# Kernel optimization log

Hardware: AMD Instinct MI355X
Metric: run time of the kernel (lower is better)

## Reference

```python
import jax, jax.numpy as jnp
import numpy as np

TAGSET = 128
START = 126
END = 127
NEG = -10000.0


def setup_inputs() -> dict:
    key = jax.random.key(0)
    k1, k2, k3 = jax.random.split(key, 3)
    B, S, T = 256, 512, TAGSET
    feats = jax.random.normal(k1, (B, S, T), dtype=jnp.float32)
    tags = jax.random.randint(k2, (B, S), 0, 126, dtype=jnp.int64)
    mask = jnp.ones((B, S), dtype=jnp.int32)
    # learned transitions with hard constraints baked in, as in __init__
    transitions = jax.random.normal(k3, (T, T), dtype=jnp.float32)
    transitions = transitions.at[START, :].set(NEG)
    transitions = transitions.at[:, END].set(NEG)
    return {"feats": feats, "tags": tags, "mask": mask, "transitions": transitions}


def _gold_score(feats, tags, mask_f, transitions):
    B, S, T = feats.shape
    tags_ext = jnp.concatenate(
        [jnp.full((B, 1), START, dtype=tags.dtype), tags], axis=1)  # (B, S+1)
    prev_t = tags_ext[:, :-1]
    cur_t = tags_ext[:, 1:]
    trans = transitions[prev_t, cur_t]                               # (B, S)
    emit = jnp.take_along_axis(feats, cur_t[:, :, None], axis=2)[..., 0]
    score = jnp.sum((trans + emit) * mask_f, axis=1)                 # (B,)
    # tag at last valid position (index mask.sum into start-prepended tags)
    lengths = jnp.sum(mask_f, axis=1).astype(jnp.int32)             # (B,)
    last_tags = jnp.take_along_axis(tags_ext, lengths[:, None].astype(tags.dtype), axis=1)[:, 0]
    return score + transitions[last_tags, END]


def _log_partition(feats, transitions):
    # NOTE: original code's mask application in the forward recursion is a
    # no-op (alpha*mask + alpha*~mask), so the recurrence runs over all steps.
    B, S, T = feats.shape
    log_alpha0 = jnp.full((B, T), NEG, dtype=feats.dtype).at[:, START].set(0.0)

    def step(log_alpha, feat_t):
        # score[b, j, k] = alpha[b, k] + transitions[j, k] + feat_t[b, j]
        s = log_alpha[:, None, :] + transitions[None, :, :] + feat_t[:, :, None]
        return jax.nn.logsumexp(s, axis=2), None

    log_alpha, _ = jax.lax.scan(step, log_alpha0, jnp.swapaxes(feats, 0, 1))
    log_alpha = log_alpha + transitions[:, END][None, :]
    return jax.nn.logsumexp(log_alpha, axis=1)                       # (B,)


def reference(feats, tags, mask, transitions):
    mask_f = mask.astype(feats.dtype)
    score = _gold_score(feats, tags, mask_f, transitions)
    log_z = _log_partition(feats, transitions)
    return -(score - log_z)  # per-example NLL, shape (B,)
```

## Files before the change

kernel.cpp:

```cpp
#include <hip/hip_runtime.h>
#include <stdint.h>

#define T_ 128
#define S_ 512
#define STARTT 126
#define ENDT 127

typedef float f32x4 __attribute__((ext_vector_type(4)));
typedef __bf16 bf16x8 __attribute__((ext_vector_type(8)));

union BFU { unsigned short s[8]; bf16x8 v; };

__device__ __forceinline__ unsigned short bf16r(float f) {
  unsigned int x = __float_as_uint(f);
  x += 0x7fffu + ((x >> 16) & 1u);
  return (unsigned short)(x >> 16);
}

__global__ __launch_bounds__(512)
void crf_fused(const float* __restrict__ feats,
               const int* __restrict__ tags,
               const int* __restrict__ mask,
               const float* __restrict__ trans,
               float* __restrict__ out)
{
  const int b    = blockIdx.x;
  const int tid  = threadIdx.x;
  const int lane = tid & 63;
  const int w    = tid >> 6;
  const int dir  = (w >= 4);
  const int wd   = w & 3;

  __shared__ __align__(16) float tstage[T_ * T_];
  __shared__ float red_s[8];
  __shared__ float red_l[8];
  __shared__ float sc_final;
  __shared__ __align__(16) unsigned short ubuf[2][2][T_];
  __shared__ float h0buf[2][2];
  __shared__ float hfF[T_], hfB[T_];
  __shared__ float cshare[2];

  const float* fb = feats + (size_t)b * (S_ * T_);

  {
    const f32x4* src = (const f32x4*)trans;
    f32x4* dst = (f32x4*)tstage;
    #pragma unroll
    for (int i = 0; i < 8; ++i) dst[tid + 512 * i] = src[tid + 512 * i];
  }
  __syncthreads();

  {
    int s = tid;
    int cur  = tags[b * S_ + s];
    int prev = (s == 0) ? STARTT : tags[b * S_ + s - 1];
    float mk = (float)mask[b * S_ + s];
    float sc = (tstage[prev * T_ + cur] + fb[s * T_ + cur]) * mk;
    float ln = mk;
    #pragma unroll
    for (int off = 32; off; off >>= 1) {
      sc += __shfl_down(sc, off);
      ln += __shfl_down(ln, off);
    }
    if (lane == 0) { red_s[w] = sc; red_l[w] = ln; }
  }
  __syncthreads();
  if (tid == 0) {
    float sc = 0.f, ln = 0.f;
    #pragma unroll
    for (int i = 0; i < 8; ++i) { sc += red_s[i]; ln += red_l[i]; }
    int L = (int)ln;
    int last = (L == 0) ? STARTT : tags[b * S_ + L - 1];
    sc_final = sc + tstage[last * T_ + ENDT];
  }

  const int n_ = lane & 15;
  const int g_ = lane >> 4;
  bf16x8 Bf0[4], Bf1[4];
  #pragma unroll
  for (int tt = 0; tt < 2; ++tt) {
    #pragma unroll
    for (int c = 0; c < 4; ++c) {
      BFU u_;
      #pragma unroll
      for (int e = 0; e < 8; ++e) {
        int kk = 32 * c + 8 * g_ + e;
        int nn = 16 * (2 * wd + tt) + n_;
        int row = dir ? kk : nn;
        int col = dir ? nn : kk;
        u_.s[e] = bf16r(__expf(tstage[row * T_ + col]));
      }
      if (tt == 0) Bf0[c] = u_.v; else Bf1[c] = u_.v;
    }
  }

  const int jf = 32 * wd + (lane & 31);
  const int rs = dir ? -T_ : T_;
  const float* fpD = fb + jf + (dir ? (511 * T_) : 0);
  float f0 = fpD[0];
  float f1 = fpD[1 * rs];
  float f2 = fpD[2 * rs];
  float f3 = fpD[3 * rs];
  float f4 = fpD[4 * rs];
  float f5 = fpD[5 * rs];
  float f6 = fpD[6 * rs];
  float f7 = fpD[7 * rs];

  float Ctot = 0.f;
  float hv;

  if (!dir) {
    float tv = tstage[jf * T_ + STARTT];
    hv = f0 + fmaxf(tv, -69.0f);
  } else {
    hv = 0.f;
  }
  {
    float uu = __expf(dir ? (hv + f0) : hv);
    if (lane < 32) ubuf[dir][1][jf] = bf16r(uu);
    if (lane == 0 && wd == 0) h0buf[dir][1] = 0.f;
  }
  f0 = fpD[8 * rs];
  asm volatile("s_waitcnt lgkmcnt(0)" ::: "memory");
  __builtin_amdgcn_s_barrier();

#define CRF_STEP(KK, FR) do {                                                  \
    const int par_ = (KK) & 1;                                                 \
    float h0p = h0buf[dir][par_];                                              \
    const unsigned short* ub_ = &ubuf[dir][par_][0];                           \
    bf16x8 A0 = *(const bf16x8*)(ub_ +       8 * g_);                          \
    bf16x8 A1 = *(const bf16x8*)(ub_ + 32 +  8 * g_);                          \
    bf16x8 A2 = *(const bf16x8*)(ub_ + 64 +  8 * g_);                          \
    bf16x8 A3 = *(const bf16x8*)(ub_ + 96 +  8 * g_);                          \
    f32x4 ac0 = {0.f, 0.f, 0.f, 0.f};                                          \
    f32x4 ac1 = ac0, ac2 = ac0, ac3 = ac0;                                     \
    ac0 = __builtin_amdgcn_mfma_f32_16x16x32_bf16(A0, Bf0[0], ac0, 0, 0, 0);   \
    ac2 = __builtin_amdgcn_mfma_f32_16x16x32_bf16(A0, Bf1[0], ac2, 0, 0, 0);   \
    ac1 = __builtin_amdgcn_mfma_f32_16x16x32_bf16(A1, Bf0[1], ac1, 0, 0, 0);   \
    ac3 = __builtin_amdgcn_mfma_f32_16x16x32_bf16(A1, Bf1[1], ac3, 0, 0, 0);   \
    ac0 = __builtin_amdgcn_mfma_f32_16x16x32_bf16(A2, Bf0[2], ac0, 0, 0, 0);   \
    ac2 = __builtin_amdgcn_mfma_f32_16x16x32_bf16(A2, Bf1[2], ac2, 0, 0, 0);   \
    ac1 = __builtin_amdgcn_mfma_f32_16x16x32_bf16(A3, Bf0[3], ac1, 0, 0, 0);   \
    ac3 = __builtin_amdgcn_mfma_f32_16x16x32_bf16(A3, Bf1[3], ac3, 0, 0, 0);   \
    float Sv = (lane & 16) ? (ac2[0] + ac3[0]) : (ac0[0] + ac1[0]);            \
    Sv = fmaxf(Sv, 1e-30f);                                                    \
    float lg_ = __logf(Sv) - h0p;                                              \
    hv = dir ? lg_ : ((FR) + lg_);                                             \
    Ctot += h0p;                                                               \
    float uu_ = __expf(dir ? (hv + (FR)) : hv);                                \
    if (lane < 32) ubuf[dir][par_ ^ 1][jf] = bf16r(uu_);                       \
    if (lane == 0 && wd == 0) h0buf[dir][par_ ^ 1] = hv;                       \
    if ((KK) + 8 <= 255) FR = fpD[((KK) + 8) * rs];                            \
    asm volatile("s_waitcnt lgkmcnt(0)" ::: "memory");                         \
    __builtin_amdgcn_s_barrier();                                              \
} while (0)

  #pragma unroll 1
  for (int k0 = 1; k0 <= 241; k0 += 8) {
    CRF_STEP(k0 + 0, f1); CRF_STEP(k0 + 1, f2); CRF_STEP(k0 + 2, f3); CRF_STEP(k0 + 3, f4);
    CRF_STEP(k0 + 4, f5); CRF_STEP(k0 + 5, f6); CRF_STEP(k0 + 6, f7); CRF_STEP(k0 + 7, f0);
  }
  CRF_STEP(249, f1); CRF_STEP(250, f2); CRF_STEP(251, f3); CRF_STEP(252, f4);
  CRF_STEP(253, f5); CRF_STEP(254, f6); CRF_STEP(255, f7);

  if (dir) {
    float h0p = h0buf[1][0];
    const unsigned short* ub_ = &ubuf[1][0][0];
    bf16x8 A0 = *(const bf16x8*)(ub_ +       8 * g_);
    bf16x8 A1 = *(const bf16x8*)(ub_ + 32 +  8 * g_);
    bf16x8 A2 = *(const bf16x8*)(ub_ + 64 +  8 * g_);
    bf16x8 A3 = *(const bf16x8*)(ub_ + 96 +  8 * g_);
    f32x4 ac0 = {0.f, 0.f, 0.f, 0.f};
    f32x4 ac1 = ac0, ac2 = ac0, ac3 = ac0;
    ac0 = __builtin_amdgcn_mfma_f32_16x16x32_bf16(A0, Bf0[0], ac0, 0, 0, 0);
    ac2 = __builtin_amdgcn_mfma_f32_16x16x32_bf16(A0, Bf1[0], ac2, 0, 0, 0);
    ac1 = __builtin_amdgcn_mfma_f32_16x16x32_bf16(A1, Bf0[1], ac1, 0, 0, 0);
    ac3 = __builtin_amdgcn_mfma_f32_16x16x32_bf16(A1, Bf1[1], ac3, 0, 0, 0);
    ac0 = __builtin_amdgcn_mfma_f32_16x16x32_bf16(A2, Bf0[2], ac0, 0, 0, 0);
    ac2 = __builtin_amdgcn_mfma_f32_16x16x32_bf16(A2, Bf1[2], ac2, 0, 0, 0);
    ac1 = __builtin_amdgcn_mfma_f32_16x16x32_bf16(A3, Bf0[3], ac1, 0, 0, 0);
    ac3 = __builtin_amdgcn_mfma_f32_16x16x32_bf16(A3, Bf1[3], ac3, 0, 0, 0);
    float Sv = (lane & 16) ? (ac2[0] + ac3[0]) : (ac0[0] + ac1[0]);
    Sv = fmaxf(Sv, 1e-30f);
    hv = __logf(Sv) - h0p;
    Ctot += h0p;
  }

  if (lane < 32) {
    if (!dir) hfF[jf] = hv; else hfB[jf] = hv;
  }
  if (tid == 0)   cshare[0] = Ctot;
  if (tid == 256) cshare[1] = Ctot;
  __syncthreads();
  if (tid < 64) {
    float a  = hfF[tid]      + hfB[tid];
    float b2 = hfF[tid + 64] + hfB[tid + 64];
    float M = fmaxf(a, b2);
    #pragma unroll
    for (int off = 32; off; off >>= 1) M = fmaxf(M, __shfl_xor(M, off));
    float sm = __expf(a - M) + __expf(b2 - M);
    #pragma unroll
    for (int off = 32; off; off >>= 1) sm += __shfl_xor(sm, off);
    if (tid == 0) {
      float logz = cshare[0] + cshare[1] + M + __logf(sm) - 10000.0f;
      out[b] = logz - sc_final;
    }
  }
#undef CRF_STEP
}

extern "C" void kernel_launch(void* const* d_in, const int* in_sizes, int n_in,
                              void* d_out, int out_size, void* d_ws, size_t ws_size,
                              hipStream_t stream) {
  const float* feats = (const float*)d_in[0];
  const int*   tags  = (const int*)d_in[1];
  const int*   mask  = (const int*)d_in[2];
  const float* trans = (const float*)d_in[3];
  float* out = (float*)d_out;
  hipLaunchKernelGGL(crf_fused, dim3(256), dim3(512), 0, stream,
                     feats, tags, mask, trans, out);
}
```

Baseline: 92.72 us.

## Merge forward/backward into same waves with power-of-two exp-domain rescaling

```diff
diff --git a/kernel.cpp b/kernel.cpp
--- a/kernel.cpp
+++ b/kernel.cpp
@@ -16,8 +16,14 @@
   x += 0x7fffu + ((x >> 16) & 1u);
   return (unsigned short)(x >> 16);
 }
-
-__global__ __launch_bounds__(512)
+__device__ __forceinline__ int expbits(float x) {
+  return (int)((__float_as_uint(x) >> 23) & 0xffu);
+}
+__device__ __forceinline__ float scalef(int k) {
+  return __uint_as_float((unsigned)(318 - k) << 23);
+}
+
+__global__ __launch_bounds__(256)
 void crf_fused(const float* __restrict__ feats,
                const int* __restrict__ tags,
                const int* __restrict__ mask,
@@ -28,17 +34,12 @@
   const int tid  = threadIdx.x;
   const int lane = tid & 63;
   const int w    = tid >> 6;
-  const int dir  = (w >= 4);
-  const int wd   = w & 3;
 
   __shared__ __align__(16) float tstage[T_ * T_];
-  __shared__ float red_s[8];
-  __shared__ float red_l[8];
+  __shared__ float red_s[4], red_l[4], redd[4];
   __shared__ float sc_final;
   __shared__ __align__(16) unsigned short ubuf[2][2][T_];
-  __shared__ float h0buf[2][2];
-  __shared__ float hfF[T_], hfB[T_];
-  __shared__ float cshare[2];
+  __shared__ __align__(8) int kbuf[2][2];
 
   const float* fb = feats + (size_t)b * (S_ * T_);
 
@@ -46,17 +47,21 @@
     const f32x4* src = (const f32x4*)trans;
     f32x4* dst = (f32x4*)tstage;
     #pragma unroll
-    for (int i = 0; i < 8; ++i) dst[tid + 512 * i] = src[tid + 512 * i];
+    for (int i = 0; i < 16; ++i) dst[tid + 256 * i] = src[tid + 256 * i];
   }
   __syncthreads();
 
   {
-    int s = tid;
-    int cur  = tags[b * S_ + s];
-    int prev = (s == 0) ? STARTT : tags[b * S_ + s - 1];
-    float mk = (float)mask[b * S_ + s];
-    float sc = (tstage[prev * T_ + cur] + fb[s * T_ + cur]) * mk;
-    float ln = mk;
+    float sc = 0.f, ln = 0.f;
+    #pragma unroll
+    for (int it = 0; it < 2; ++it) {
+      int s = tid + 256 * it;
+      int cur  = tags[b * S_ + s];
+      int prev = (s == 0) ? STARTT : tags[b * S_ + s - 1];
+      float mk = (float)mask[b * S_ + s];
+      sc += (tstage[prev * T_ + cur] + fb[s * T_ + cur]) * mk;
+      ln += mk;
+    }
     #pragma unroll
     for (int off = 32; off; off >>= 1) {
       sc += __shfl_down(sc, off);
@@ -68,7 +73,7 @@
   if (tid == 0) {
     float sc = 0.f, ln = 0.f;
     #pragma unroll
-    for (int i = 0; i < 8; ++i) { sc += red_s[i]; ln += red_l[i]; }
+    for (int i = 0; i < 4; ++i) { sc += red_s[i]; ln += red_l[i]; }
     int L = (int)ln;
     int last = (L == 0) ? STARTT : tags[b * S_ + L - 1];
     sc_final = sc + tstage[last * T_ + ENDT];
@@ -76,137 +81,164 @@
 
   const int n_ = lane & 15;
   const int g_ = lane >> 4;
-  bf16x8 Bf0[4], Bf1[4];
-  #pragma unroll
-  for (int tt = 0; tt < 2; ++tt) {
-    #pragma unroll
-    for (int c = 0; c < 4; ++c) {
-      BFU u_;
-      #pragma unroll
-      for (int e = 0; e < 8; ++e) {
-        int kk = 32 * c + 8 * g_ + e;
-        int nn = 16 * (2 * wd + tt) + n_;
-        int row = dir ? kk : nn;
-        int col = dir ? nn : kk;
-        u_.s[e] = bf16r(__expf(tstage[row * T_ + col]));
-      }
-      if (tt == 0) Bf0[c] = u_.v; else Bf1[c] = u_.v;
-    }
-  }
-
-  const int jf = 32 * wd + (lane & 31);
-  const int rs = dir ? -T_ : T_;
-  const float* fpD = fb + jf + (dir ? (511 * T_) : 0);
-  float f0 = fpD[0];
-  float f1 = fpD[1 * rs];
-  float f2 = fpD[2 * rs];
-  float f3 = fpD[3 * rs];
-  float f4 = fpD[4 * rs];
-  float f5 = fpD[5 * rs];
-  float f6 = fpD[6 * rs];
-  float f7 = fpD[7 * rs];
-
-  float Ctot = 0.f;
-  float hv;
-
-  if (!dir) {
-    float tv = tstage[jf * T_ + STARTT];
-    hv = f0 + fmaxf(tv, -69.0f);
-  } else {
-    hv = 0.f;
-  }
-  {
-    float uu = __expf(dir ? (hv + f0) : hv);
-    if (lane < 32) ubuf[dir][1][jf] = bf16r(uu);
-    if (lane == 0 && wd == 0) h0buf[dir][1] = 0.f;
-  }
-  f0 = fpD[8 * rs];
+  bf16x8 BF0[4], BF1[4], BB0[4], BB1[4];
+
+#define BUILDFRAG(DST, ROW_IS_K, TT) do {                                      \
+    _Pragma("unroll")                                                          \
+    for (int c = 0; c < 4; ++c) {                                              \
+      BFU u_;                                                                  \
+      _Pragma("unroll")                                                        \
+      for (int e = 0; e < 8; ++e) {                                            \
+        int kk = 32 * c + 8 * g_ + e;                                          \
+        int nn = 16 * (2 * w + (TT)) + n_;                                     \
+        int row = (ROW_IS_K) ? kk : nn;                                        \
+        int col = (ROW_IS_K) ? nn : kk;                                        \
+        u_.s[e] = bf16r(__expf(tstage[row * T_ + col]));                       \
+      }                                                                        \
+      DST[c] = u_.v;                                                           \
+    }                                                                          \
+  } while (0)
+
+  BUILDFRAG(BF0, 0, 0);  BUILDFRAG(BF1, 0, 1);
+  BUILDFRAG(BB0, 1, 0);  BUILDFRAG(BB1, 1, 1);
+#undef BUILDFRAG
+
+  const int jf = 32 * w + (lane & 31);
+  const bool lhalf = (lane < 32);
+  const bool selhi = (lane & 16) != 0;
+  const float* fpF = fb + jf;
+  const float* fpB = fb + jf + 511 * T_;
+  float fF0 = fpF[0 * T_], fF1 = fpF[1 * T_], fF2 = fpF[2 * T_], fF3 = fpF[3 * T_];
+  float fF4 = fpF[4 * T_], fF5 = fpF[5 * T_], fF6 = fpF[6 * T_], fF7 = fpF[7 * T_];
+  float fB0 = fpB[0], fB1 = fpB[-1 * T_], fB2 = fpB[-2 * T_], fB3 = fpB[-3 * T_];
+  float fB4 = fpB[-4 * T_], fB5 = fpB[-5 * T_], fB6 = fpB[-6 * T_], fB7 = fpB[-7 * T_];
+
+  int ksumF = 0, ksumB = 0;
+  float lastF = 0.f;
+
+  {
+    float trS = tstage[jf * T_ + STARTT];
+    float uF = __expf(fF0 + trS);
+    float uB = __expf(fB0);
+    if (lhalf) {
+      ubuf[0][1][jf] = bf16r(uF);
+      ubuf[1][1][jf] = bf16r(uB);
+    }
+    if (tid == 0) {
+      int2 kw; kw.x = expbits(uF); kw.y = expbits(uB);
+      *(int2*)&kbuf[1][0] = kw;
+    }
+    fF0 = fpF[8 * T_];
+    fB0 = fpB[-8 * T_];
+  }
   asm volatile("s_waitcnt lgkmcnt(0)" ::: "memory");
   __builtin_amdgcn_s_barrier();
 
-#define CRF_STEP(KK, FR) do {                                                  \
-    const int par_ = (KK) & 1;                                                 \
-    float h0p = h0buf[dir][par_];                                              \
-    const unsigned short* ub_ = &ubuf[dir][par_][0];                           \
-    bf16x8 A0 = *(const bf16x8*)(ub_ +       8 * g_);                          \
-    bf16x8 A1 = *(const bf16x8*)(ub_ + 32 +  8 * g_);                          \
-    bf16x8 A2 = *(const bf16x8*)(ub_ + 64 +  8 * g_);                          \
-    bf16x8 A3 = *(const bf16x8*)(ub_ + 96 +  8 * g_);                          \
-    f32x4 ac0 = {0.f, 0.f, 0.f, 0.f};                                          \
-    f32x4 ac1 = ac0, ac2 = ac0, ac3 = ac0;                                     \
-    ac0 = __builtin_amdgcn_mfma_f32_16x16x32_bf16(A0, Bf0[0], ac0, 0, 0, 0);   \
-    ac2 = __builtin_amdgcn_mfma_f32_16x16x32_bf16(A0, Bf1[0], ac2, 0, 0, 0);   \
-    ac1 = __builtin_amdgcn_mfma_f32_16x16x32_bf16(A1, Bf0[1], ac1, 0, 0, 0);   \
-    ac3 = __builtin_amdgcn_mfma_f32_16x16x32_bf16(A1, Bf1[1], ac3, 0, 0, 0);   \
-    ac0 = __builtin_amdgcn_mfma_f32_16x16x32_bf16(A2, Bf0[2], ac0, 0, 0, 0);   \
-    ac2 = __builtin_amdgcn_mfma_f32_16x16x32_bf16(A2, Bf1[2], ac2, 0, 0, 0);   \
-    ac1 = __builtin_amdgcn_mfma_f32_16x16x32_bf16(A3, Bf0[3], ac1, 0, 0, 0);   \
-    ac3 = __builtin_amdgcn_mfma_f32_16x16x32_bf16(A3, Bf1[3], ac3, 0, 0, 0);   \
-    float Sv = (lane & 16) ? (ac2[0] + ac3[0]) : (ac0[0] + ac1[0]);            \
-    Sv = fmaxf(Sv, 1e-30f);                                                    \
-    float lg_ = __logf(Sv) - h0p;                                              \
-    hv = dir ? lg_ : ((FR) + lg_);                                             \
-    Ctot += h0p;                                                               \
-    float uu_ = __expf(dir ? (hv + (FR)) : hv);                                \
-    if (lane < 32) ubuf[dir][par_ ^ 1][jf] = bf16r(uu_);                       \
-    if (lane == 0 && wd == 0) h0buf[dir][par_ ^ 1] = hv;                       \
-    if ((KK) + 8 <= 255) FR = fpD[((KK) + 8) * rs];                            \
+#define STEP_BODY(KK, FF, FB, DOPF) do {                                       \
+    const int par = (KK) & 1;                                                  \
+    int2 kk2 = *(const int2*)&kbuf[par][0];                                    \
+    const unsigned short* uf  = &ubuf[0][par][0];                              \
+    const unsigned short* ub2 = &ubuf[1][par][0];                              \
+    bf16x8 AF0 = *(const bf16x8*)(uf  +       8 * g_);                         \
+    bf16x8 AF1 = *(const bf16x8*)(uf  + 32 +  8 * g_);                         \
+    bf16x8 AF2 = *(const bf16x8*)(uf  + 64 +  8 * g_);                         \
+    bf16x8 AF3 = *(const bf16x8*)(uf  + 96 +  8 * g_);                         \
+    bf16x8 AB0 = *(const bf16x8*)(ub2 +       8 * g_);                         \
+    bf16x8 AB1 = *(const bf16x8*)(ub2 + 32 +  8 * g_);                         \
+    bf16x8 AB2 = *(const bf16x8*)(ub2 + 64 +  8 * g_);                         \
+    bf16x8 AB3 = *(const bf16x8*)(ub2 + 96 +  8 * g_);                         \
+    float mF = __expf(FF) * scalef(kk2.x);                                     \
+    float mB = __expf(FB) * scalef(kk2.y);                                     \
+    f32x4 aF0 = {0.f,0.f,0.f,0.f}; f32x4 aF1 = aF0, aF2 = aF0, aF3 = aF0;      \
+    f32x4 aB0 = aF0, aB1 = aF0, aB2 = aF0, aB3 = aF0;                          \
+    aF0 = __builtin_amdgcn_mfma_f32_16x16x32_bf16(AF0, BF0[0], aF0, 0, 0, 0);  \
+    aF2 = __builtin_amdgcn_mfma_f32_16x16x32_bf16(AF0, BF1[0], aF2, 0, 0, 0);  \
+    aF1 = __builtin_amdgcn_mfma_f32_16x16x32_bf16(AF1, BF0[1], aF1, 0, 0, 0);  \
+    aF3 = __builtin_amdgcn_mfma_f32_16x16x32_bf16(AF1, BF1[1], aF3, 0, 0, 0);  \
+    aF0 = __builtin_amdgcn_mfma_f32_16x16x32_bf16(AF2, BF0[2], aF0, 0, 0, 0);  \
+    aF2 = __builtin_amdgcn_mfma_f32_16x16x32_bf16(AF2, BF1[2], aF2, 0, 0, 0);  \
+    aF1 = __builtin_amdgcn_mfma_f32_16x16x32_bf16(AF3, BF0[3], aF1, 0, 0, 0);  \
+    aF3 = __builtin_amdgcn_mfma_f32_16x16x32_bf16(AF3, BF1[3], aF3, 0, 0, 0);  \
+    aB0 = __builtin_amdgcn_mfma_f32_16x16x32_bf16(AB0, BB0[0], aB0, 0, 0, 0);  \
+    aB2 = __builtin_amdgcn_mfma_f32_16x16x32_bf16(AB0, BB1[0], aB2, 0, 0, 0);  \
+    aB1 = __builtin_amdgcn_mfma_f32_16x16x32_bf16(AB1, BB0[1], aB1, 0, 0, 0);  \
+    aB3 = __builtin_amdgcn_mfma_f32_16x16x32_bf16(AB1, BB1[1], aB3, 0, 0, 0);  \
+    aB0 = __builtin_amdgcn_mfma_f32_16x16x32_bf16(AB2, BB0[2], aB0, 0, 0, 0);  \
+    aB2 = __builtin_amdgcn_mfma_f32_16x16x32_bf16(AB2, BB1[2], aB2, 0, 0, 0);  \
+    aB1 = __builtin_amdgcn_mfma_f32_16x16x32_bf16(AB3, BB0[3], aB1, 0, 0, 0);  \
+    aB3 = __builtin_amdgcn_mfma_f32_16x16x32_bf16(AB3, BB1[3], aB3, 0, 0, 0);  \
+    float SvF = selhi ? (aF2[0] + aF3[0]) : (aF0[0] + aF1[0]);                 \
+    float uFn = SvF * mF;                                                      \
+    float SvB = selhi ? (aB2[0] + aB3[0]) : (aB0[0] + aB1[0]);                 \
+    float uBn = SvB * mB;                                                      \
+    if (lhalf) {                                                               \
+      ubuf[0][par ^ 1][jf] = bf16r(uFn);                                       \
+      ubuf[1][par ^ 1][jf] = bf16r(uBn);                                       \
+    }                                                                          \
+    if (tid == 0) {                                                            \
+      int2 kw; kw.x = expbits(uFn); kw.y = expbits(uBn);                       \
+      *(int2*)&kbuf[par ^ 1][0] = kw;                                          \
+    }                                                                          \
+    ksumF += kk2.x; ksumB += kk2.y;                                            \
+    lastF = uFn;                                                               \
+    if (DOPF) {                                                                \
+      FF = fpF[((KK) + 8) * T_];                                               \
+      FB = fpB[-(((KK) + 8) * T_)];                                            \
+    }                                                                          \
     asm volatile("s_waitcnt lgkmcnt(0)" ::: "memory");                         \
     __builtin_amdgcn_s_barrier();                                              \
-} while (0)
+  } while (0)
+
+#define STEP(KK, FF, FB)  STEP_BODY(KK, FF, FB, 1)
+#define STEPN(KK, FF, FB) STEP_BODY(KK, FF, FB, 0)
 
   #pragma unroll 1
-  for (int k0 = 1; k0 <= 241; k0 += 8) {
-    CRF_STEP(k0 + 0, f1); CRF_STEP(k0 + 1, f2); CRF_STEP(k0 + 2, f3); CRF_STEP(k0 + 3, f4);
-    CRF_STEP(k0 + 4, f5); CRF_STEP(k0 + 5, f6); CRF_STEP(k0 + 6, f7); CRF_STEP(k0 + 7, f0);
-  }
-  CRF_STEP(249, f1); CRF_STEP(250, f2); CRF_STEP(251, f3); CRF_STEP(252, f4);
-  CRF_STEP(253, f5); CRF_STEP(254, f6); CRF_STEP(255, f7);
-
-  if (dir) {
-    float h0p = h0buf[1][0];
-    const unsigned short* ub_ = &ubuf[1][0][0];
-    bf16x8 A0 = *(const bf16x8*)(ub_ +       8 * g_);
-    bf16x8 A1 = *(const bf16x8*)(ub_ + 32 +  8 * g_);
-    bf16x8 A2 = *(const bf16x8*)(ub_ + 64 +  8 * g_);
-    bf16x8 A3 = *(const bf16x8*)(ub_ + 96 +  8 * g_);
-    f32x4 ac0 = {0.f, 0.f, 0.f, 0.f};
-    f32x4 ac1 = ac0, ac2 = ac0, ac3 = ac0;
-    ac0 = __builtin_amdgcn_mfma_f32_16x16x32_bf16(A0, Bf0[0], ac0, 0, 0, 0);
-    ac2 = __builtin_amdgcn_mfma_f32_16x16x32_bf16(A0, Bf1[0], ac2, 0, 0, 0);
-    ac1 = __builtin_amdgcn_mfma_f32_16x16x32_bf16(A1, Bf0[1], ac1, 0, 0, 0);
-    ac3 = __builtin_amdgcn_mfma_f32_16x16x32_bf16(A1, Bf1[1], ac3, 0, 0, 0);
-    ac0 = __builtin_amdgcn_mfma_f32_16x16x32_bf16(A2, Bf0[2], ac0, 0, 0, 0);
-    ac2 = __builtin_amdgcn_mfma_f32_16x16x32_bf16(A2, Bf1[2], ac2, 0, 0, 0);
-    ac1 = __builtin_amdgcn_mfma_f32_16x16x32_bf16(A3, Bf0[3], ac1, 0, 0, 0);
-    ac3 = __builtin_amdgcn_mfma_f32_16x16x32_bf16(A3, Bf1[3], ac3, 0, 0, 0);
-    float Sv = (lane & 16) ? (ac2[0] + ac3[0]) : (ac0[0] + ac1[0]);
-    Sv = fmaxf(Sv, 1e-30f);
-    hv = __logf(Sv) - h0p;
-    Ctot += h0p;
-  }
-
-  if (lane < 32) {
-    if (!dir) hfF[jf] = hv; else hfB[jf] = hv;
-  }
-  if (tid == 0)   cshare[0] = Ctot;
-  if (tid == 256) cshare[1] = Ctot;
+  for (int k0 = 1; k0 <= 233; k0 += 8) {
+    STEP(k0 + 0, fF1, fB1); STEP(k0 + 1, fF2, fB2);
+    STEP(k0 + 2, fF3, fB3); STEP(k0 + 3, fF4, fB4);
+    STEP(k0 + 4, fF5, fB5); STEP(k0 + 5, fF6, fB6);
+    STEP(k0 + 6, fF7, fB7); STEP(k0 + 7, fF0, fB0);
+  }
+  STEP (241, fF1, fB1); STEP (242, fF2, fB2); STEP (243, fF3, fB3);
+  STEP (244, fF4, fB4); STEP (245, fF5, fB5); STEP (246, fF6, fB6);
+  STEP (247, fF7, fB7); STEPN(248, fF0, fB0);
+  STEPN(249, fF1, fB1); STEPN(250, fF2, fB2); STEPN(251, fF3, fB3);
+  STEPN(252, fF4, fB4); STEPN(253, fF5, fB5); STEPN(254, fF6, fB6);
+  STEPN(255, fF7, fB7);
+
+#undef STEP
+#undef STEPN
+#undef STEP_BODY
+
+  {
+    const unsigned short* ub2 = &ubuf[1][0][0];
+    bf16x8 AB0 = *(const bf16x8*)(ub2 +       8 * g_);
+    bf16x8 AB1 = *(const bf16x8*)(ub2 + 32 +  8 * g_);
+    bf16x8 AB2 = *(const bf16x8*)(ub2 + 64 +  8 * g_);
+    bf16x8 AB3 = *(const bf16x8*)(ub2 + 96 +  8 * g_);
+    f32x4 aB0 = {0.f,0.f,0.f,0.f}; f32x4 aB1 = aB0, aB2 = aB0, aB3 = aB0;
+    aB0 = __builtin_amdgcn_mfma_f32_16x16x32_bf16(AB0, BB0[0], aB0, 0, 0, 0);
+    aB2 = __builtin_amdgcn_mfma_f32_16x16x32_bf16(AB0, BB1[0], aB2, 0, 0, 0);
+    aB1 = __builtin_amdgcn_mfma_f32_16x16x32_bf16(AB1, BB0[1], aB1, 0, 0, 0);
+    aB3 = __builtin_amdgcn_mfma_f32_16x16x32_bf16(AB1, BB1[1], aB3, 0, 0, 0);
+    aB0 = __builtin_amdgcn_mfma_f32_16x16x32_bf16(AB2, BB0[2], aB0, 0, 0, 0);
+    aB2 = __builtin_amdgcn_mfma_f32_16x16x32_bf16(AB2, BB1[2], aB2, 0, 0, 0);
+    aB1 = __builtin_amdgcn_mfma_f32_16x16x32_bf16(AB3, BB0[3], aB1, 0, 0, 0);
+    aB3 = __builtin_amdgcn_mfma_f32_16x16x32_bf16(AB3, BB1[3], aB3, 0, 0, 0);
+    float SvB = selhi ? (aB2[0] + aB3[0]) : (aB0[0] + aB1[0]);
+    float d = lhalf ? (lastF * 0x1p-64f) * (SvB * 0x1p-64f) : 0.f;
+    #pragma unroll
+    for (int off = 32; off; off >>= 1) d += __shfl_down(d, off);
+    if (lane == 0) redd[w] = d;
+  }
   __syncthreads();
-  if (tid < 64) {
-    float a  = hfF[tid]      + hfB[tid];
-    float b2 = hfF[tid + 64] + hfB[tid + 64];
-    float M = fmaxf(a, b2);
-    #pragma unroll
-    for (int off = 32; off; off >>= 1) M = fmaxf(M, __shfl_xor(M, off));
-    float sm = __expf(a - M) + __expf(b2 - M);
-    #pragma unroll
-    for (int off = 32; off; off >>= 1) sm += __shfl_xor(sm, off);
-    if (tid == 0) {
-      float logz = cshare[0] + cshare[1] + M + __logf(sm) - 10000.0f;
-      out[b] = logz - sc_final;
-    }
-  }
-#undef CRF_STEP
+  if (tid == 0) {
+    float dot = redd[0] + redd[1] + redd[2] + redd[3];
+    float logz = __logf(dot)
+               + (float)(ksumF + ksumB - 2 * 255 * 191 + 128) * 0.69314718056f
+               - 10000.0f;
+    out[b] = logz - sc_final;
+  }
 }
 
 extern "C" void kernel_launch(void* const* d_in, const int* in_sizes, int n_in,
@@ -217,6 +249,6 @@
   const int*   mask  = (const int*)d_in[2];
   const float* trans = (const float*)d_in[3];
   float* out = (float*)d_out;
-  hipLaunchKernelGGL(crf_fused, dim3(256), dim3(512), 0, stream,
+  hipLaunchKernelGGL(crf_fused, dim3(256), dim3(256), 0, stream,
                      feats, tags, mask, trans, out);
 }
```

After: 96.63 us. 4.2% more time.

## Run each CRF direction in a single wave using bpermute and exponent scaling

Applied to the files above, without the earlier changes.

```diff
diff --git a/kernel.cpp b/kernel.cpp
--- a/kernel.cpp
+++ b/kernel.cpp
@@ -9,6 +9,7 @@
 typedef float f32x4 __attribute__((ext_vector_type(4)));
 typedef __bf16 bf16x8 __attribute__((ext_vector_type(8)));
 
+union ABU { int i[4]; bf16x8 v; };
 union BFU { unsigned short s[8]; bf16x8 v; };
 
 __device__ __forceinline__ unsigned short bf16r(float f) {
@@ -16,8 +17,16 @@
   x += 0x7fffu + ((x >> 16) & 1u);
   return (unsigned short)(x >> 16);
 }
-
-__global__ __launch_bounds__(512)
+__device__ __forceinline__ float scalef(int k) {
+  return __uint_as_float((unsigned)(318 - k) << 23);
+}
+__device__ __forceinline__ unsigned cvt_pk_bf16(float lo, float hi) {
+  unsigned r;
+  asm("v_cvt_pk_bf16_f32 %0, %1, %2" : "=v"(r) : "v"(lo), "v"(hi));
+  return r;
+}
+
+__global__ __launch_bounds__(128, 1)
 void crf_fused(const float* __restrict__ feats,
                const int* __restrict__ tags,
                const int* __restrict__ mask,
@@ -28,17 +37,15 @@
   const int tid  = threadIdx.x;
   const int lane = tid & 63;
   const int w    = tid >> 6;
-  const int dir  = (w >= 4);
-  const int wd   = w & 3;
+  const int dir  = w;
+  const int cl   = lane & 15;
+  const int g    = lane >> 4;
 
   __shared__ __align__(16) float tstage[T_ * T_];
-  __shared__ float red_s[8];
-  __shared__ float red_l[8];
+  __shared__ float red_s[2], red_l[2];
+  __shared__ float fin_uf[T_], fin_w[T_];
+  __shared__ int   kls[2];
   __shared__ float sc_final;
-  __shared__ __align__(16) unsigned short ubuf[2][2][T_];
-  __shared__ float h0buf[2][2];
-  __shared__ float hfF[T_], hfB[T_];
-  __shared__ float cshare[2];
 
   const float* fb = feats + (size_t)b * (S_ * T_);
 
@@ -46,17 +53,21 @@
     const f32x4* src = (const f32x4*)trans;
     f32x4* dst = (f32x4*)tstage;
     #pragma unroll
-    for (int i = 0; i < 8; ++i) dst[tid + 512 * i] = src[tid + 512 * i];
+    for (int i = 0; i < 32; ++i) dst[tid + 128 * i] = src[tid + 128 * i];
   }
   __syncthreads();
 
   {
-    int s = tid;
-    int cur  = tags[b * S_ + s];
-    int prev = (s == 0) ? STARTT : tags[b * S_ + s - 1];
-    float mk = (float)mask[b * S_ + s];
-    float sc = (tstage[prev * T_ + cur] + fb[s * T_ + cur]) * mk;
-    float ln = mk;
+    float sc = 0.f, ln = 0.f;
+    #pragma unroll
+    for (int it = 0; it < 4; ++it) {
+      int s = tid + 128 * it;
+      int cur  = tags[b * S_ + s];
+      int prev = s ? tags[b * S_ + s - 1] : STARTT;
+      float mk = (float)mask[b * S_ + s];
+      sc += (tstage[prev * T_ + cur] + fb[s * T_ + cur]) * mk;
+      ln += mk;
+    }
     #pragma unroll
     for (int off = 32; off; off >>= 1) {
       sc += __shfl_down(sc, off);
@@ -66,147 +77,173 @@
   }
   __syncthreads();
   if (tid == 0) {
-    float sc = 0.f, ln = 0.f;
-    #pragma unroll
-    for (int i = 0; i < 8; ++i) { sc += red_s[i]; ln += red_l[i]; }
+    float sc = red_s[0] + red_s[1];
+    float ln = red_l[0] + red_l[1];
     int L = (int)ln;
-    int last = (L == 0) ? STARTT : tags[b * S_ + L - 1];
+    int last = L ? tags[b * S_ + L - 1] : STARTT;
     sc_final = sc + tstage[last * T_ + ENDT];
   }
 
-  const int n_ = lane & 15;
-  const int g_ = lane >> 4;
-  bf16x8 Bf0[4], Bf1[4];
+  bf16x8 Bfr[8][4];
   #pragma unroll
-  for (int tt = 0; tt < 2; ++tt) {
+  for (int t = 0; t < 8; ++t) {
     #pragma unroll
     for (int c = 0; c < 4; ++c) {
-      BFU u_;
+      BFU bu;
       #pragma unroll
       for (int e = 0; e < 8; ++e) {
-        int kk = 32 * c + 8 * g_ + e;
-        int nn = 16 * (2 * wd + tt) + n_;
-        int row = dir ? kk : nn;
-        int col = dir ? nn : kk;
-        u_.s[e] = bf16r(__expf(tstage[row * T_ + col]));
+        int ktag = 32 * (e >> 1) + 16 * (e & 1) + 4 * c + g;
+        int nn = 16 * t + cl;
+        float tv = dir ? tstage[ktag * T_ + nn] : tstage[nn * T_ + ktag];
+        bu.s[e] = bf16r(__expf(tv));
       }
-      if (tt == 0) Bf0[c] = u_.v; else Bf1[c] = u_.v;
-    }
-  }
-
-  const int jf = 32 * wd + (lane & 31);
+      Bfr[t][c] = bu.v;
+    }
+  }
+
+  int bp0 = (0 + g) * 4, bp1 = (4 + g) * 4, bp2 = (8 + g) * 4, bp3 = (12 + g) * 4;
+
   const int rs = dir ? -T_ : T_;
-  const float* fpD = fb + jf + (dir ? (511 * T_) : 0);
-  float f0 = fpD[0];
-  float f1 = fpD[1 * rs];
-  float f2 = fpD[2 * rs];
-  float f3 = fpD[3 * rs];
-  float f4 = fpD[4 * rs];
-  float f5 = fpD[5 * rs];
-  float f6 = fpD[6 * rs];
-  float f7 = fpD[7 * rs];
-
-  float Ctot = 0.f;
-  float hv;
+  const float* frow1 = fb + (dir ? 510 * T_ : 1 * T_) + cl;
+  float fr0[8], fr1[8], fr2[8], fr3[8];
+  #pragma unroll
+  for (int t = 0; t < 8; ++t) {
+    fr0[t] = frow1[0 * rs + 16 * t];
+    fr1[t] = frow1[1 * rs + 16 * t];
+    fr2[t] = frow1[2 * rs + 16 * t];
+    fr3[t] = frow1[3 * rs + 16 * t];
+  }
+  const float* fpl = frow1 + 4 * rs;
+
+  float u8v[8];
+  {
+    const float* f0p = fb + (dir ? 511 * T_ : 0) + cl;
+    #pragma unroll
+    for (int t = 0; t < 8; ++t) {
+      float fv = f0p[16 * t];
+      float tv = dir ? 0.f : tstage[(16 * t + cl) * T_ + STARTT];
+      u8v[t] = __expf(fv + tv);
+    }
+  }
+  int kexp = (__builtin_amdgcn_readlane((int)__float_as_uint(u8v[0]), 0) >> 23) & 255;
+  int ksum = kexp;
+  float scale = scalef(kexp);
+
+  ABU af[4];
+  {
+    unsigned Q0 = cvt_pk_bf16(u8v[0], u8v[1]);
+    unsigned Q1 = cvt_pk_bf16(u8v[2], u8v[3]);
+    unsigned Q2 = cvt_pk_bf16(u8v[4], u8v[5]);
+    unsigned Q3 = cvt_pk_bf16(u8v[6], u8v[7]);
+    af[0].i[0] = __builtin_amdgcn_ds_bpermute(bp0, (int)Q0);
+    af[0].i[1] = __builtin_amdgcn_ds_bpermute(bp0, (int)Q1);
+    af[0].i[2] = __builtin_amdgcn_ds_bpermute(bp0, (int)Q2);
+    af[0].i[3] = __builtin_amdgcn_ds_bpermute(bp0, (int)Q3);
+    af[1].i[0] = __builtin_amdgcn_ds_bpermute(bp1, (int)Q0);
+    af[1].i[1] = __builtin_amdgcn_ds_bpermute(bp1, (int)Q1);
+    af[1].i[2] = __builtin_amdgcn_ds_bpermute(bp1, (int)Q2);
+    af[1].i[3] = __builtin_amdgcn_ds_bpermute(bp1, (int)Q3);
+    af[2].i[0] = __builtin_amdgcn_ds_bpermute(bp2, (int)Q0);
+    af[2].i[1] = __builtin_amdgcn_ds_bpermute(bp2, (int)Q1);
+    af[2].i[2] = __builtin_amdgcn_ds_bpermute(bp2, (int)Q2);
+    af[2].i[3] = __builtin_amdgcn_ds_bpermute(bp2, (int)Q3);
+    af[3].i[0] = __builtin_amdgcn_ds_bpermute(bp3, (int)Q0);
+    af[3].i[1] = __builtin_amdgcn_ds_bpermute(bp3, (int)Q1);
+    af[3].i[2] = __builtin_amdgcn_ds_bpermute(bp3, (int)Q2);
+    af[3].i[3] = __builtin_amdgcn_ds_bpermute(bp3, (int)Q3);
+  }
+
+#define STEP(FR, UPD, PF) do {                                                   \
+    f32x4 z4 = {0.f, 0.f, 0.f, 0.f};                                             \
+    float S8[8];                                                                  \
+    _Pragma("unroll")                                                             \
+    for (int t = 0; t < 8; ++t) {                                                 \
+      f32x4 aA = __builtin_amdgcn_mfma_f32_16x16x32_bf16(af[0].v, Bfr[t][0], z4, 0, 0, 0); \
+      aA = __builtin_amdgcn_mfma_f32_16x16x32_bf16(af[1].v, Bfr[t][1], aA, 0, 0, 0);       \
+      f32x4 aB = __builtin_amdgcn_mfma_f32_16x16x32_bf16(af[2].v, Bfr[t][2], z4, 0, 0, 0); \
+      aB = __builtin_amdgcn_mfma_f32_16x16x32_bf16(af[3].v, Bfr[t][3], aB, 0, 0, 0);       \
+      S8[t] = aA[0] + aB[0];                                                      \
+    }                                                                             \
+    _Pragma("unroll")                                                             \
+    for (int t = 0; t < 8; ++t) u8v[t] = S8[t] * scale * __expf(FR[t]);           \
+    if (UPD) {                                                                    \
+      kexp = (__builtin_amdgcn_readlane((int)__float_as_uint(u8v[0]), 0) >> 23) & 255; \
+      ksum += kexp;                                                               \
+      scale = scalef(kexp);                                                       \
+    }                                                                             \
+    unsigned Q0 = cvt_pk_bf16(u8v[0], u8v[1]);                                    \
+    unsigned Q1 = cvt_pk_bf16(u8v[2], u8v[3]);                                    \
+    unsigned Q2 = cvt_pk_bf16(u8v[4], u8v[5]);                                    \
+    unsigned Q3 = cvt_pk_bf16(u8v[6], u8v[7]);                                    \
+    af[0].i[0] = __builtin_amdgcn_ds_bpermute(bp0, (int)Q0);                      \
+    af[0].i[1] = __builtin_amdgcn_ds_bpermute(bp0, (int)Q1);                      \
+    af[0].i[2] = __builtin_amdgcn_ds_bpermute(bp0, (int)Q2);                      \
+    af[0].i[3] = __builtin_amdgcn_ds_bpermute(bp0, (int)Q3);                      \
+    af[1].i[0] = __builtin_amdgcn_ds_bpermute(bp1, (int)Q0);                      \
+    af[1].i[1] = __builtin_amdgcn_ds_bpermute(bp1, (int)Q1);                      \
+    af[1].i[2] = __builtin_amdgcn_ds_bpermute(bp1, (int)Q2);                      \
+    af[1].i[3] = __builtin_amdgcn_ds_bpermute(bp1, (int)Q3);                      \
+    af[2].i[0] = __builtin_amdgcn_ds_bpermute(bp2, (int)Q0);                      \
+    af[2].i[1] = __builtin_amdgcn_ds_bpermute(bp2, (int)Q1);                      \
+    af[2].i[2] = __builtin_amdgcn_ds_bpermute(bp2, (int)Q2);                      \
+    af[2].i[3] = __builtin_amdgcn_ds_bpermute(bp2, (int)Q3);                      \
+    af[3].i[0] = __builtin_amdgcn_ds_bpermute(bp3, (int)Q0);                      \
+    af[3].i[1] = __builtin_amdgcn_ds_bpermute(bp3, (int)Q1);                      \
+    af[3].i[2] = __builtin_amdgcn_ds_bpermute(bp3, (int)Q2);                      \
+    af[3].i[3] = __builtin_amdgcn_ds_bpermute(bp3, (int)Q3);                      \
+    if (PF) {                                                                     \
+      _Pragma("unroll")                                                           \
+      for (int t = 0; t < 8; ++t) FR[t] = fpl[16 * t];                            \
+      fpl += rs;                                                                  \
+    }                                                                             \
+  } while (0)
+
+  #pragma unroll 1
+  for (int k0 = 0; k0 < 63; ++k0) {
+    STEP(fr0, 1, 1); STEP(fr1, 1, 1); STEP(fr2, 1, 1); STEP(fr3, 1, 1);
+  }
+  STEP(fr0, 1, 1);
+  STEP(fr1, 1, 1);
+  STEP(fr2, 0, 0);
+#undef STEP
 
   if (!dir) {
-    float tv = tstage[jf * T_ + STARTT];
-    hv = f0 + fmaxf(tv, -69.0f);
+    if (lane < 16) {
+      #pragma unroll
+      for (int t = 0; t < 8; ++t) fin_uf[16 * t + cl] = u8v[t];
+    }
+    if (lane == 0) kls[0] = ksum;
   } else {
-    hv = 0.f;
-  }
-  {
-    float uu = __expf(dir ? (hv + f0) : hv);
-    if (lane < 32) ubuf[dir][1][jf] = bf16r(uu);
-    if (lane == 0 && wd == 0) h0buf[dir][1] = 0.f;
-  }
-  f0 = fpD[8 * rs];
-  asm volatile("s_waitcnt lgkmcnt(0)" ::: "memory");
-  __builtin_amdgcn_s_barrier();
-
-#define CRF_STEP(KK, FR) do {                                                  \
-    const int par_ = (KK) & 1;                                                 \
-    float h0p = h0buf[dir][par_];                                              \
-    const unsigned short* ub_ = &ubuf[dir][par_][0];                           \
-    bf16x8 A0 = *(const bf16x8*)(ub_ +       8 * g_);                          \
-    bf16x8 A1 = *(const bf16x8*)(ub_ + 32 +  8 * g_);                          \
-    bf16x8 A2 = *(const bf16x8*)(ub_ + 64 +  8 * g_);                          \
-    bf16x8 A3 = *(const bf16x8*)(ub_ + 96 +  8 * g_);                          \
-    f32x4 ac0 = {0.f, 0.f, 0.f, 0.f};                                          \
-    f32x4 ac1 = ac0, ac2 = ac0, ac3 = ac0;                                     \
-    ac0 = __builtin_amdgcn_mfma_f32_16x16x32_bf16(A0, Bf0[0], ac0, 0, 0, 0);   \
-    ac2 = __builtin_amdgcn_mfma_f32_16x16x32_bf16(A0, Bf1[0], ac2, 0, 0, 0);   \
-    ac1 = __builtin_amdgcn_mfma_f32_16x16x32_bf16(A1, Bf0[1], ac1, 0, 0, 0);   \
-    ac3 = __builtin_amdgcn_mfma_f32_16x16x32_bf16(A1, Bf1[1], ac3, 0, 0, 0);   \
-    ac0 = __builtin_amdgcn_mfma_f32_16x16x32_bf16(A2, Bf0[2], ac0, 0, 0, 0);   \
-    ac2 = __builtin_amdgcn_mfma_f32_16x16x32_bf16(A2, Bf1[2], ac2, 0, 0, 0);   \
-    ac1 = __builtin_amdgcn_mfma_f32_16x16x32_bf16(A3, Bf0[3], ac1, 0, 0, 0);   \
-    ac3 = __builtin_amdgcn_mfma_f32_16x16x32_bf16(A3, Bf1[3], ac3, 0, 0, 0);   \
-    float Sv = (lane & 16) ? (ac2[0] + ac3[0]) : (ac0[0] + ac1[0]);            \
-    Sv = fmaxf(Sv, 1e-30f);                                                    \
-    float lg_ = __logf(Sv) - h0p;                                              \
-    hv = dir ? lg_ : ((FR) + lg_);                                             \
-    Ctot += h0p;                                                               \
-    float uu_ = __expf(dir ? (hv + (FR)) : hv);                                \
-    if (lane < 32) ubuf[dir][par_ ^ 1][jf] = bf16r(uu_);                       \
-    if (lane == 0 && wd == 0) h0buf[dir][par_ ^ 1] = hv;                       \
-    if ((KK) + 8 <= 255) FR = fpD[((KK) + 8) * rs];                            \
-    asm volatile("s_waitcnt lgkmcnt(0)" ::: "memory");                         \
-    __builtin_amdgcn_s_barrier();                                              \
-} while (0)
-
-  #pragma unroll 1
-  for (int k0 = 1; k0 <= 241; k0 += 8) {
-    CRF_STEP(k0 + 0, f1); CRF_STEP(k0 + 1, f2); CRF_STEP(k0 + 2, f3); CRF_STEP(k0 + 3, f4);
-    CRF_STEP(k0 + 4, f5); CRF_STEP(k0 + 5, f6); CRF_STEP(k0 + 6, f7); CRF_STEP(k0 + 7, f0);
-  }
-  CRF_STEP(249, f1); CRF_STEP(250, f2); CRF_STEP(251, f3); CRF_STEP(252, f4);
-  CRF_STEP(253, f5); CRF_STEP(254, f6); CRF_STEP(255, f7);
-
-  if (dir) {
-    float h0p = h0buf[1][0];
-    const unsigned short* ub_ = &ubuf[1][0][0];
-    bf16x8 A0 = *(const bf16x8*)(ub_ +       8 * g_);
-    bf16x8 A1 = *(const bf16x8*)(ub_ + 32 +  8 * g_);
-    bf16x8 A2 = *(const bf16x8*)(ub_ + 64 +  8 * g_);
-    bf16x8 A3 = *(const bf16x8*)(ub_ + 96 +  8 * g_);
-    f32x4 ac0 = {0.f, 0.f, 0.f, 0.f};
-    f32x4 ac1 = ac0, ac2 = ac0, ac3 = ac0;
-    ac0 = __builtin_amdgcn_mfma_f32_16x16x32_bf16(A0, Bf0[0], ac0, 0, 0, 0);
-    ac2 = __builtin_amdgcn_mfma_f32_16x16x32_bf16(A0, Bf1[0], ac2, 0, 0, 0);
-    ac1 = __builtin_amdgcn_mfma_f32_16x16x32_bf16(A1, Bf0[1], ac1, 0, 0, 0);
-    ac3 = __builtin_amdgcn_mfma_f32_16x16x32_bf16(A1, Bf1[1], ac3, 0, 0, 0);
-    ac0 = __builtin_amdgcn_mfma_f32_16x16x32_bf16(A2, Bf0[2], ac0, 0, 0, 0);
-    ac2 = __builtin_amdgcn_mfma_f32_16x16x32_bf16(A2, Bf1[2], ac2, 0, 0, 0);
-    ac1 = __builtin_amdgcn_mfma_f32_16x16x32_bf16(A3, Bf0[3], ac1, 0, 0, 0);
-    ac3 = __builtin_amdgcn_mfma_f32_16x16x32_bf16(A3, Bf1[3], ac3, 0, 0, 0);
-    float Sv = (lane & 16) ? (ac2[0] + ac3[0]) : (ac0[0] + ac1[0]);
-    Sv = fmaxf(Sv, 1e-30f);
-    hv = __logf(Sv) - h0p;
-    Ctot += h0p;
-  }
-
-  if (lane < 32) {
-    if (!dir) hfF[jf] = hv; else hfB[jf] = hv;
-  }
-  if (tid == 0)   cshare[0] = Ctot;
-  if (tid == 256) cshare[1] = Ctot;
+    f32x4 z4 = {0.f, 0.f, 0.f, 0.f};
+    float S8[8];
+    #pragma unroll
+    for (int t = 0; t < 8; ++t) {
+      f32x4 aA = __builtin_amdgcn_mfma_f32_16x16x32_bf16(af[0].v, Bfr[t][0], z4, 0, 0, 0);
+      aA = __builtin_amdgcn_mfma_f32_16x16x32_bf16(af[1].v, Bfr[t][1], aA, 0, 0, 0);
+      f32x4 aB = __builtin_amdgcn_mfma_f32_16x16x32_bf16(af[2].v, Bfr[t][2], z4, 0, 0, 0);
+      aB = __builtin_amdgcn_mfma_f32_16x16x32_bf16(af[3].v, Bfr[t][3], aB, 0, 0, 0);
+      S8[t] = aA[0] + aB[0];
+    }
+    if (lane < 16) {
+      #pragma unroll
+      for (int t = 0; t < 8; ++t) fin_w[16 * t + cl] = S8[t];
+    }
+    if (lane == 0) kls[1] = ksum;
+  }
   __syncthreads();
+
   if (tid < 64) {
-    float a  = hfF[tid]      + hfB[tid];
-    float b2 = hfF[tid + 64] + hfB[tid + 64];
-    float M = fmaxf(a, b2);
-    #pragma unroll
-    for (int off = 32; off; off >>= 1) M = fmaxf(M, __shfl_xor(M, off));
-    float sm = __expf(a - M) + __expf(b2 - M);
-    #pragma unroll
-    for (int off = 32; off; off >>= 1) sm += __shfl_xor(sm, off);
+    float d = (fin_uf[tid] * 0x1p-64f) * (fin_w[tid] * 0x1p-64f)
+            + (fin_uf[tid + 64] * 0x1p-64f) * (fin_w[tid + 64] * 0x1p-64f);
+    #pragma unroll
+    for (int off = 32; off; off >>= 1) d += __shfl_down(d, off);
     if (tid == 0) {
-      float logz = cshare[0] + cshare[1] + M + __logf(sm) - 10000.0f;
+      float logz = __logf(d)
+                 + (float)(kls[0] + kls[1] - 2 * 255 * 191 + 128) * 0.6931471805599453f
+                 - 10000.0f;
       out[b] = logz - sc_final;
     }
   }
-#undef CRF_STEP
 }
 
 extern "C" void kernel_launch(void* const* d_in, const int* in_sizes, int n_in,
@@ -217,6 +254,6 @@
   const int*   mask  = (const int*)d_in[2];
   const float* trans = (const float*)d_in[3];
   float* out = (float*)d_out;
-  hipLaunchKernelGGL(crf_fused, dim3(256), dim3(512), 0, stream,
+  hipLaunchKernelGGL(crf_fused, dim3(256), dim3(128), 0, stream,
                      feats, tags, mask, trans, out);
 }
```

After: 125.0 us. +34.8%, slower.
